# Optimization experiments

Hardware: AMD Instinct MI355X
Metric: run time of the kernel (lower is better)

## Reference

```python
import jax, jax.numpy as jnp
import numpy as np
from jax import lax

S, B, W = 128, 64, 16          # sent_len, batch, word_len
V, CV = 50000, 100             # word vocab, char vocab
WE, CE, FN, CK = 300, 30, 4, 3 # word emb dim, char emb dim, char filter num, char kernel
C = 512                        # cnn_out_channel
NT = 20                        # number of tags
NL = 3                         # number of GLU conv layers
PAD = 0


def setup_inputs() -> dict:
    key = jax.random.key(0)
    ks = jax.random.split(key, 16)
    words = jax.random.randint(ks[0], (S, B), 1, V)          # no pads -> full CRF mask
    chars = jax.random.randint(ks[1], (B, S, W), 1, CV)
    tags = jax.random.randint(ks[2], (S, B), 0, NT)
    word_emb = jax.random.normal(ks[3], (V, WE), jnp.float32) * 0.1
    char_emb = jax.random.normal(ks[4], (CV, CE), jnp.float32) * 0.1
    char_cnn_w = jax.random.normal(ks[5], (CE * FN, 1, CK), jnp.float32) * 0.1  # grouped conv, groups=CE
    char_cnn_b = jax.random.normal(ks[6], (CE * FN,), jnp.float32) * 0.01
    lin_w = jax.random.normal(ks[7], (WE + CE * FN, C), jnp.float32) * 0.05
    lin_b = jax.random.normal(ks[8], (C,), jnp.float32) * 0.01
    conv_w = jax.random.normal(ks[9], (NL, 2 * C, C, 3), jnp.float32) * 0.03
    conv_b = jax.random.normal(ks[10], (NL, 2 * C), jnp.float32) * 0.01
    fc_w = jax.random.normal(ks[11], (C, NT), jnp.float32) * 0.05
    fc_b = jax.random.normal(ks[12], (NT,), jnp.float32) * 0.01
    crf_start = jax.random.normal(ks[13], (NT,), jnp.float32) * 0.1
    crf_end = jax.random.normal(ks[14], (NT,), jnp.float32) * 0.1
    crf_trans = jax.random.normal(ks[15], (NT, NT), jnp.float32) * 0.1
    return dict(words=words, chars=chars, tags=tags, word_emb=word_emb, char_emb=char_emb,
                char_cnn_w=char_cnn_w, char_cnn_b=char_cnn_b, lin_w=lin_w, lin_b=lin_b,
                conv_w=conv_w, conv_b=conv_b, fc_w=fc_w, fc_b=fc_b,
                crf_start=crf_start, crf_end=crf_end, crf_trans=crf_trans)


def _emissions(words, chars, word_emb, char_emb, char_cnn_w, char_cnn_b,
               lin_w, lin_b, conv_w, conv_b, fc_w, fc_b):
    s, b = words.shape
    # word embeddings: [S,B,WE]
    emb_out = word_emb[words]
    # char embeddings + batched grouped char-CNN (replaces the python loop over sent positions)
    ch = char_emb[chars]                                   # [B,S,W,CE]
    ch = ch.reshape(b * s, W, CE).transpose(0, 2, 1)       # [B*S, CE, W]
    co = lax.conv_general_dilated(ch, char_cnn_w, (1,), 'VALID',
                                  dimension_numbers=('NCH', 'OIH', 'NCH'),
                                  feature_group_count=CE)
    co = co + char_cnn_b[None, :, None]                    # [B*S, CE*FN, W-CK+1]
    cf = co.max(axis=2).reshape(b, s, CE * FN).transpose(1, 0, 2)  # [S,B,120]
    word_features = jnp.concatenate([emb_out, cf], axis=2)  # [S,B,420]
    # gated-CNN (GLU) encoder
    h = word_features @ lin_w + lin_b                      # [S,B,C]
    h = jnp.transpose(h, (1, 2, 0))                        # [B,C,S]
    scale = jnp.sqrt(jnp.asarray(0.5, h.dtype))
    for l in range(conv_w.shape[0]):
        c = lax.conv_general_dilated(h, conv_w[l], (1,), ((1, 1),),
                                     dimension_numbers=('NCH', 'OIH', 'NCH'))
        c = c + conv_b[l][None, :, None]                   # [B,2C,S]
        a, g = jnp.split(c, 2, axis=1)
        h = (a * jax.nn.sigmoid(g) + h) * scale            # GLU + residual + scale
    enc = jnp.transpose(h, (2, 0, 1))                      # [S,B,C]
    emis = enc @ fc_w + fc_b                               # [S,B,NT]
    mask = (words != PAD)                                  # [S,B]
    return emis, mask


def _crf_nll(emis, tags, mask, crf_start, crf_end, crf_trans):
    s, b, nt = emis.shape
    maskf = mask.astype(emis.dtype)
    bi = jnp.arange(b)
    # numerator: score of the gold path
    emis_sc = jnp.take_along_axis(emis, tags[:, :, None], axis=2)[..., 0]  # [S,B]
    trans_sc = crf_trans[tags[:-1], tags[1:]]                              # [S-1,B]
    num = crf_start[tags[0]] + emis_sc[0] + ((trans_sc + emis_sc[1:]) * maskf[1:]).sum(0)
    last_idx = mask.sum(0).astype(jnp.int32) - 1
    num = num + crf_end[tags[last_idx, bi]]
    # denominator: forward algorithm (sequential DP over time)
    alpha0 = crf_start[None, :] + emis[0]                  # [B,NT]
    def step(alpha, xs):
        e_t, m_t = xs
        nxt = jax.nn.logsumexp(alpha[:, :, None] + crf_trans[None] + e_t[:, None, :], axis=1)
        return jnp.where(m_t[:, None], nxt, alpha), None
    alpha, _ = lax.scan(step, alpha0, (emis[1:], mask[1:]))
    logz = jax.nn.logsumexp(alpha + crf_end[None, :], axis=1)
    return -(num - logz).sum()


def _viterbi(emis, mask, crf_start, crf_end, crf_trans):
    s, b, nt = emis.shape
    bi = jnp.arange(b)
    ident = jnp.broadcast_to(jnp.arange(nt)[None, :], (b, nt))
    score0 = crf_start[None, :] + emis[0]                  # [B,NT]
    def step(score, xs):
        e_t, m_t = xs
        brd = score[:, :, None] + crf_trans[None]          # [B,NT_prev,NT_cur]
        bp = jnp.argmax(brd, axis=1)                       # [B,NT]
        nxt = jnp.max(brd, axis=1) + e_t
        score = jnp.where(m_t[:, None], nxt, score)
        bp = jnp.where(m_t[:, None], bp, ident)
        return score, bp
    final, bps = lax.scan(step, score0, (emis[1:], mask[1:]))  # bps [S-1,B,NT]
    last_tag = jnp.argmax(final + crf_end[None, :], axis=1)    # [B]
    def back(tag, bp):
        prev = bp[bi, tag]
        return prev, tag
    first_tag, rest = lax.scan(back, last_tag, bps, reverse=True)  # rest: tags at 1..S-1
    return jnp.concatenate([first_tag[None], rest], axis=0).astype(jnp.int32)  # [S,B]


def reference(words, chars, tags, word_emb, char_emb, char_cnn_w, char_cnn_b,
              lin_w, lin_b, conv_w, conv_b, fc_w, fc_b, crf_start, crf_end, crf_trans):
    emis, mask = _emissions(words, chars, word_emb, char_emb, char_cnn_w, char_cnn_b,
                            lin_w, lin_b, conv_w, conv_b, fc_w, fc_b)
    crf_out = _viterbi(emis, mask, crf_start, crf_end, crf_trans)
    crf_loss = _crf_nll(emis, tags, mask, crf_start, crf_end, crf_trans)
    return crf_out, crf_loss
```

## Files before the change

kernel.cpp:

```cpp
#include <hip/hip_runtime.h>
#include <math.h>

typedef unsigned short ushort_t;
typedef short bf16x8 __attribute__((ext_vector_type(8)));
typedef float f32x4 __attribute__((ext_vector_type(4)));
typedef unsigned short u16x8 __attribute__((ext_vector_type(8)));

#define S_ 128
#define B_ 64
#define W_ 16
#define CE_ 30
#define FN_ 4
#define WE_ 300
#define FEAT_ 420
#define C_ 512
#define NT_ 20
#define KL_ 448

#define LOG2E_ 1.44269504088896340736f
#define LN2_   0.69314718055994530942f

#define WF_OFF   0
#define EM_OFF   3440640
#define NLL_OFF  3604480
#define H0_OFF   3604608
#define HBUF_F   2129920
#define H1_OFF   (H0_OFF + HBUF_F)
#define WS_OFF   (H1_OFF + HBUF_F)
#define WSP_F    2359296
#define LW_OFF   (WS_OFF + WSP_F)
#define FS_OFF   (LW_OFF + 114688)
#define FW_OFF   (FS_OFF + 1835008)
#define WLAYER   (1024*1536)

__device__ __forceinline__ float b2f(ushort_t h) {
    unsigned u = ((unsigned)h) << 16;
    float f; __builtin_memcpy(&f, &u, 4); return f;
}
__device__ __forceinline__ ushort_t f2b(float f) {
    unsigned u; __builtin_memcpy(&u, &f, 4);
    unsigned r = (u + 0x7FFFu + ((u >> 16) & 1u)) >> 16;
    return (ushort_t)r;
}
__device__ __forceinline__ void gload16(const void* g, void* l) {
    __builtin_amdgcn_global_load_lds((const __attribute__((address_space(1))) void*)g,
                                     (__attribute__((address_space(3))) void*)l,
                                     16, 0, 0);
}

__global__ void k_word_gather(const int* __restrict__ words,
                              const float* __restrict__ word_emb,
                              float* __restrict__ wf) {
    int n = blockIdx.x;
    int wid = words[n];
    int t = threadIdx.x;
    if (t < WE_ / 4) {
        const float4* src = (const float4*)(word_emb + (size_t)wid * WE_);
        float4* dst = (float4*)(wf + (size_t)n * FEAT_);
        dst[t] = src[t];
    }
}

__global__ void k_char_cnn(const int* __restrict__ chars,
                           const float* __restrict__ char_emb,
                           const float* __restrict__ cw,
                           const float* __restrict__ cb,
                           float* __restrict__ wf) {
    int n = blockIdx.x;
    int b = n >> 7;
    int s = n & 127;
    __shared__ int cidx[W_];
    int t = threadIdx.x;
    if (t < W_) cidx[t] = chars[n * W_ + t];
    __syncthreads();
    if (t < CE_ * FN_) {
        int g = t >> 2;
        float w0 = cw[t*3+0], w1 = cw[t*3+1], w2 = cw[t*3+2];
        float x[W_];
        #pragma unroll
        for (int j = 0; j < W_; ++j) x[j] = char_emb[cidx[j] * CE_ + g];
        float m = -INFINITY;
        #pragma unroll
        for (int j = 0; j < W_ - 2; ++j) {
            float v = x[j]*w0 + x[j+1]*w1 + x[j+2]*w2;
            m = fmaxf(m, v);
        }
        wf[(size_t)(s * B_ + b) * FEAT_ + WE_ + t] = m + cb[t];
    }
}

__global__ void k_split_w(const float* __restrict__ conv_w,
                          ushort_t* __restrict__ Wt) {
    size_t i = (size_t)blockIdx.x * 256 + threadIdx.x;
    int ci = (int)(i & 511);
    int kr = (int)((i >> 9) % 3);
    size_t lo_ = i / 1536;
    Wt[i] = f2b(conv_w[lo_ * 1536 + (size_t)ci * 3 + kr]);
}

__global__ void k_split_lw(const float* __restrict__ lin_w,
                           ushort_t* __restrict__ Lh) {
    int k = blockIdx.x;
    int c = threadIdx.x;
    float v = (k < FEAT_) ? lin_w[(size_t)k * C_ + c] : 0.f;
    Lh[(size_t)c * KL_ + k] = f2b(v);
}

__global__ void k_split_wf(const float* __restrict__ wf,
                           ushort_t* __restrict__ Fh) {
    int np = blockIdx.x;
    int b = np >> 7, s = np & 127;
    const float* src = wf + (size_t)(s * B_ + b) * FEAT_;
    int t = threadIdx.x;
    #pragma unroll
    for (int r = 0; r < 2; ++r) {
        int k = t + r * 224;
        float v = (k < FEAT_) ? src[k] : 0.f;
        Fh[(size_t)np * KL_ + k] = f2b(v);
    }
}

__global__ void k_split_fw(const float* __restrict__ fc_w, float* __restrict__ fwT) {
    int idx = blockIdx.x * 256 + threadIdx.x;
    if (idx < NT_ * C_) {
        int j = idx >> 9, c = idx & 511;
        fwT[idx] = fc_w[(size_t)c * NT_ + j];
    }
}

__global__ void k_zero_pad(ushort_t* b0, ushort_t* b1) {
    ushort_t* buf = blockIdx.y ? b1 : b0;
    int b = blockIdx.x;
    int t = threadIdx.x;
    unsigned* r0 = (unsigned*)(buf + ((size_t)b * 130 + 0) * 512);
    unsigned* r1 = (unsigned*)(buf + ((size_t)b * 130 + 129) * 512);
    r0[t] = 0u; r1[t] = 0u;
}

__global__ __launch_bounds__(256) void k_lin_gemm(
    const ushort_t* __restrict__ Lh, const ushort_t* __restrict__ Fh,
    const float* __restrict__ lb, ushort_t* __restrict__ Oh)
{
    __shared__ short lds[8192];
    short* AhS = lds;
    short* BhS = lds + 4096;

    const int bid = blockIdx.x;
    const int c0 = (bid & 3) << 7;
    const int n0 = (bid >> 2) << 7;
    const int t = threadIdx.x;
    const int w = t >> 6;
    const int lane = t & 63;
    const int wr = w >> 1, wc = w & 1;

    const int srow0 = (w << 5) + (lane >> 2);
    const int srow1 = srow0 + 16;
    const int j0 = (lane & 3) ^ ((srow0 >> 1) & 3);
    const int j1 = (lane & 3) ^ ((srow1 >> 1) & 3);
    const size_t aoff0 = (size_t)(c0 + srow0) * KL_ + j0 * 8;
    const size_t aoff1 = (size_t)(c0 + srow1) * KL_ + j1 * 8;
    const size_t boff0 = (size_t)(n0 + srow0) * KL_ + j0 * 8;
    const size_t boff1 = (size_t)(n0 + srow1) * KL_ + j1 * 8;
    const int wofs = w << 10;

    const int lr = lane & 15, kg = lane >> 4;
    int aro[4], bro[4];
    #pragma unroll
    for (int m = 0; m < 4; ++m) { int r = (wr << 6) + (m << 4) + lr; aro[m] = (r << 5) + ((kg ^ ((r >> 1) & 3)) << 3); }
    #pragma unroll
    for (int n = 0; n < 4; ++n) { int r = (wc << 6) + (n << 4) + lr; bro[n] = (r << 5) + ((kg ^ ((r >> 1) & 3)) << 3); }

    f32x4 acc[4][4];
    #pragma unroll
    for (int m = 0; m < 4; ++m)
        #pragma unroll
        for (int n = 0; n < 4; ++n) acc[m][n] = (f32x4){0.f, 0.f, 0.f, 0.f};

    for (int k0 = 0; k0 < KL_; k0 += 32) {
        gload16(Lh + aoff0 + k0, AhS + wofs);
        gload16(Lh + aoff1 + k0, AhS + wofs + 512);
        gload16(Fh + boff0 + k0, BhS + wofs);
        gload16(Fh + boff1 + k0, BhS + wofs + 512);
        __syncthreads();
        bf16x8 avh[4], bvh[4];
        #pragma unroll
        for (int m = 0; m < 4; ++m) avh[m] = *(const bf16x8*)(AhS + aro[m]);
        #pragma unroll
        for (int n = 0; n < 4; ++n) bvh[n] = *(const bf16x8*)(BhS + bro[n]);
        #pragma unroll
        for (int m = 0; m < 4; ++m)
            #pragma unroll
            for (int n = 0; n < 4; ++n)
                acc[m][n] = __builtin_amdgcn_mfma_f32_16x16x32_bf16(avh[m], bvh[n], acc[m][n], 0, 0, 0);
        __syncthreads();
    }

    #pragma unroll
    for (int m = 0; m < 4; ++m) {
        const int c = c0 + (wr << 6) + (m << 4) + (kg << 2);
        float4 bb = *(const float4*)(lb + c);
        #pragma unroll
        for (int n = 0; n < 4; ++n) {
            const int np = n0 + (wc << 6) + (n << 4) + lr;
            const int b = np >> 7, s = np & 127;
            ushort4 h4;
            h4.x = f2b(acc[m][n][0] + bb.x);
            h4.y = f2b(acc[m][n][1] + bb.y);
            h4.z = f2b(acc[m][n][2] + bb.z);
            h4.w = f2b(acc[m][n][3] + bb.w);
            *(ushort4*)(Oh + ((size_t)b * 130 + s + 1) * 512 + c) = h4;
        }
    }
}

__global__ __launch_bounds__(256) void k_conv_gemm(
    const ushort_t* __restrict__ Wt, const ushort_t* __restrict__ Ht,
    const float* __restrict__ cb,
    ushort_t* __restrict__ Ot)
{
    __shared__ short lds[17408];
    short* AS = lds;
    short* BS = lds + 12288;
    float* g_lds = (float*)lds;

    const int bid  = blockIdx.x;
    const int co0  = (bid & 7) << 6;
    const int b    = bid >> 3;
    const int t    = threadIdx.x;
    const int w    = t >> 6;
    const int lane = t & 63;
    const int wr   = w >> 1;
    const int wc   = w & 1;

    const int srow0 = (w << 5) + (lane >> 2);
    const int srow1 = srow0 + 16;
    const int j0 = (lane & 3) ^ ((srow0 >> 1) & 3);
    const int j1 = (lane & 3) ^ ((srow1 >> 1) & 3);
    const int coA0 = (srow0 < 64) ? (co0 + srow0) : (512 + co0 + srow0 - 64);
    const int coA1 = (srow1 < 64) ? (co0 + srow1) : (512 + co0 + srow1 - 64);
    const size_t aoff0 = (size_t)coA0 * 1536 + j0 * 8;
    const size_t aoff1 = (size_t)coA1 * 1536 + j1 * 8;
    const int lrow = lane >> 2;
    const int wofs = w << 10;

    const int lr = lane & 15, kg = lane >> 4;
    int aro[4];
    #pragma unroll
    for (int m = 0; m < 4; ++m) { int r = (wr << 6) + (m << 4) + lr; aro[m] = (r << 5) + ((kg ^ ((r >> 1) & 3)) << 3); }
    int bro[3][4];
    #pragma unroll
    for (int kr = 0; kr < 3; ++kr)
        #pragma unroll
        for (int n = 0; n < 4; ++n) {
            int r = (wc << 6) + (n << 4) + lr + kr;
            bro[kr][n] = (r << 5) + ((kg ^ ((r >> 1) & 3)) << 3);
        }

    f32x4 acc[4][4];
    #pragma unroll
    for (int m = 0; m < 4; ++m)
        #pragma unroll
        for (int n = 0; n < 4; ++n) acc[m][n] = (f32x4){0.f, 0.f, 0.f, 0.f};

    for (int ci0 = 0; ci0 < 512; ci0 += 32) {
        #pragma unroll
        for (int kr = 0; kr < 3; ++kr) {
            gload16(Wt + aoff0 + kr * 512 + ci0, AS + kr * 4096 + wofs);
            gload16(Wt + aoff1 + kr * 512 + ci0, AS + kr * 4096 + wofs + 512);
        }
        for (int i = w; i < 9; i += 4) {
            const int rr = (i << 4) + lrow;
            const int sl = (lane & 3) ^ ((rr >> 1) & 3);
            gload16(Ht + ((size_t)b * 130 + rr) * 512 + ci0 + sl * 8, BS + (i << 9));
        }
        __syncthreads();
        #pragma unroll
        for (int kr = 0; kr < 3; ++kr) {
            const short* A_h = AS + kr * 4096;
            bf16x8 avh[4], bvh[4];
            #pragma unroll
            for (int m = 0; m < 4; ++m) avh[m] = *(const bf16x8*)(A_h + aro[m]);
            #pragma unroll
            for (int n = 0; n < 4; ++n) bvh[n] = *(const bf16x8*)(BS + bro[kr][n]);
            #pragma unroll
            for (int m = 0; m < 4; ++m)
                #pragma unroll
                for (int n = 0; n < 4; ++n)
                    acc[m][n] = __builtin_amdgcn_mfma_f32_16x16x32_bf16(avh[m], bvh[n], acc[m][n], 0, 0, 0);
        }
        __syncthreads();
    }

    const float rs = 0.70710678118654752f;
    if (wr == 1) {
        #pragma unroll
        for (int m = 0; m < 4; ++m) {
            const int co_l = (m << 4) + (kg << 2);
            float4 bg = *(const float4*)(cb + 512 + co0 + co_l);
            #pragma unroll
            for (int n = 0; n < 4; ++n) {
                const int s_l = (wc << 6) + (n << 4) + lr;
                float4 gv;
                gv.x = acc[m][n][0] + bg.x;
                gv.y = acc[m][n][1] + bg.y;
                gv.z = acc[m][n][2] + bg.z;
                gv.w = acc[m][n][3] + bg.w;
                *(float4*)&g_lds[s_l * 68 + co_l] = gv;
            }
        }
    }
    __syncthreads();
    if (wr == 0) {
        #pragma unroll
        for (int m = 0; m < 4; ++m) {
            const int co_l = (m << 4) + (kg << 2);
            float4 ba = *(const float4*)(cb + co0 + co_l);
            #pragma unroll
            for (int n = 0; n < 4; ++n) {
                const int s_l = (wc << 6) + (n << 4) + lr;
                float4 gv = *(const float4*)&g_lds[s_l * 68 + co_l];
                size_t dst = ((size_t)b * 130 + s_l + 1) * 512 + co0 + co_l;
                ushort4 rh = *(const ushort4*)(Ht + dst);
                float a0 = acc[m][n][0] + ba.x, g0 = gv.x;
                float a1 = acc[m][n][1] + ba.y, g1 = gv.y;
                float a2 = acc[m][n][2] + ba.z, g2 = gv.z;
                float a3 = acc[m][n][3] + ba.w, g3 = gv.w;
                ushort4 h4;
                h4.x = f2b((a0 / (1.f + expf(-g0)) + b2f(rh.x)) * rs);
                h4.y = f2b((a1 / (1.f + expf(-g1)) + b2f(rh.y)) * rs);
                h4.z = f2b((a2 / (1.f + expf(-g2)) + b2f(rh.z)) * rs);
                h4.w = f2b((a3 / (1.f + expf(-g3)) + b2f(rh.w)) * rs);
                *(ushort4*)(Ot + dst) = h4;
            }
        }
    }
}

__global__ __launch_bounds__(256) void k_emis3(const ushort_t* __restrict__ hh,
                                               const float* __restrict__ fwT,
                                               const float* __restrict__ fc_b,
                                               float* __restrict__ emis) {
    __shared__ short hlds[16 * 520];
    __shared__ float wlds[20 * 516];
    const int b  = blockIdx.y;
    const int sc = blockIdx.x;
    const int t  = threadIdx.x;
    const int w  = t >> 6, lane = t & 63;

    #pragma unroll
    for (int i = 0; i < 4; ++i) {
        int r = w * 4 + i;
        gload16(hh + ((size_t)b * 130 + sc * 16 + r + 1) * 512 + lane * 8,
                hlds + r * 520);
    }
    for (int idx = t; idx < 20 * 128; idx += 256) {
        int j = idx >> 7, cq = (idx & 127) << 2;
        *(float4*)&wlds[j * 516 + cq] = *(const float4*)(fwT + j * 512 + cq);
    }
    __syncthreads();

    #pragma unroll
    for (int pass = 0; pass < 2; ++pass) {
        int slot = t + pass * 256;
        if (slot < 16 * NT_) {
            int r = slot / NT_, j = slot - r * NT_;
            const short* hp = hlds + r * 520;
            const float* wp = wlds + j * 516;
            float acc = 0.f;
            for (int c0 = 0; c0 < 512; c0 += 8) {
                u16x8 hv = *(const u16x8*)(hp + c0);
                float4 w0 = *(const float4*)(wp + c0);
                float4 w1 = *(const float4*)(wp + c0 + 4);
                acc += b2f(hv[0])*w0.x + b2f(hv[1])*w0.y + b2f(hv[2])*w0.z + b2f(hv[3])*w0.w
                     + b2f(hv[4])*w1.x + b2f(hv[5])*w1.y + b2f(hv[6])*w1.z + b2f(hv[7])*w1.w;
            }
            int s = sc * 16 + r;
            emis[((size_t)s * B_ + b) * NT_ + j] = acc + fc_b[j];
        }
    }
}

#define VMAX(a, b) __builtin_elementwise_max((a), (b))
#define MAX20T(mx, a0, a1, a2, a3, a4) \
    { f32x4 mv_ = VMAX(VMAX(VMAX(a0, a1), VMAX(a2, a3)), a4); \
      mx = fmaxf(fmaxf(mv_[0], mv_[1]), fmaxf(mv_[2], mv_[3])); }
#define SEL(ov, oi, av, ai, bv2, bi2) \
    { bool g_ = (bv2) > (av); ov = g_ ? (bv2) : (av); oi = g_ ? (bi2) : (ai); }
#define ARGMAX20(best, bi, v0, v1, v2, v3, v4) \
    { float p0v,p1v,p2v,p3v,p4v,p5v,p6v,p7v,p8v,p9v; \
      int   p0i,p1i,p2i,p3i,p4i,p5i,p6i,p7i,p8i,p9i; \
      SEL(p0v,p0i, v0[0],0,  v0[1],1);  SEL(p1v,p1i, v0[2],2,  v0[3],3); \
      SEL(p2v,p2i, v1[0],4,  v1[1],5);  SEL(p3v,p3i, v1[2],6,  v1[3],7); \
      SEL(p4v,p4i, v2[0],8,  v2[1],9);  SEL(p5v,p5i, v2[2],10, v2[3],11); \
      SEL(p6v,p6i, v3[0],12, v3[1],13); SEL(p7v,p7i, v3[2],14, v3[3],15); \
      SEL(p8v,p8i, v4[0],16, v4[1],17); SEL(p9v,p9i, v4[2],18, v4[3],19); \
      float q0v,q1v,q2v,q3v,q4v; int q0i,q1i,q2i,q3i,q4i; \
      SEL(q0v,q0i,p0v,p0i,p1v,p1i); SEL(q1v,q1i,p2v,p2i,p3v,p3i); \
      SEL(q2v,q2i,p4v,p4i,p5v,p5i); SEL(q3v,q3i,p6v,p6i,p7v,p7i); \
      SEL(q4v,q4i,p8v,p8i,p9v,p9i); \
      float r0v,r1v; int r0i,r1i; \
      SEL(r0v,r0i,q0v,q0i,q1v,q1i); SEL(r1v,r1i,q2v,q2i,q3v,q3i); \
      float s0v; int s0i; \
      SEL(s0v,s0i,r0v,r0i,r1v,r1i); \
      SEL(best,bi,s0v,s0i,q4v,q4i); }
#define EXPC(d, s) d[0]=__builtin_amdgcn_exp2f(s[0]*LOG2E_); d[1]=__builtin_amdgcn_exp2f(s[1]*LOG2E_); \
                   d[2]=__builtin_amdgcn_exp2f(s[2]*LOG2E_); d[3]=__builtin_amdgcn_exp2f(s[3]*LOG2E_)
#define LGKM0() asm volatile("s_waitcnt lgkmcnt(0)" ::: "memory")

__global__ __launch_bounds__(256) void k_crf(const float* __restrict__ emis,
                                             const int* __restrict__ words,
                                             const int* __restrict__ tags,
                                             const float* __restrict__ tstart,
                                             const float* __restrict__ tend,
                                             const float* __restrict__ ttrans,
                                             float* __restrict__ nll,
                                             float* __restrict__ out) {
    __shared__ float e_lds[S_ * NT_];
    __shared__ float pe_lds[S_ * NT_];
    __shared__ int   P_lds[S_ * NT_];
    __shared__ float brA[32], brB[32], brC[32], brD[32];
    __shared__ float Fv[NT_], Gv[NT_], a63[NT_], g63[NT_];
    __shared__ float CfL, CbL;
    __shared__ int tag63L;
    const int b = blockIdx.x;
    const int t = threadIdx.x;
    const int w = t >> 6;
    const int ln = t & 63;

    for (int idx = t; idx < S_ * NT_; idx += 256) {
        int tt = idx / NT_, j = idx - tt * NT_;
        float ev = emis[((size_t)tt * B_ + b) * NT_ + j];
        e_lds[idx] = ev;
        pe_lds[idx] = __builtin_amdgcn_exp2f(ev * LOG2E_);
    }
    __syncthreads();

    unsigned long long mlo = __ballot(words[ln * B_ + b] != 0);
    unsigned long long mhi = __ballot(words[(64 + ln) * B_ + b] != 0);
    const bool act = ln < NT_;
    const int jc = act ? ln : 0;
    float part = 0.f;

    #define MBIT(tt) ((((tt) < 64 ? (mlo >> (tt)) : (mhi >> ((tt) - 64))) & 1ull) != 0)

    if (w == 0) {
        for (int tt = ln; tt < S_; tt += 64) {
            int tgc = tags[tt * B_ + b];
            bool m = MBIT(tt);
            if (tt == 0) {
                part += tstart[tgc] + e_lds[tgc];
            } else if (m) {
                int tgp = tags[(tt - 1) * B_ + b];
                part += ttrans[tgp * NT_ + tgc] + e_lds[tt * NT_ + tgc];
            }
        }
        #pragma unroll
        for (int o = 32; o >= 1; o >>= 1) part += __shfl_down(part, o);

        f32x4 t0, t1, t2, t3, t4;
        #define LDTC(v, q) v = (f32x4){ ttrans[(4*(q)+0)*NT_ + jc], ttrans[(4*(q)+1)*NT_ + jc], \
                                        ttrans[(4*(q)+2)*NT_ + jc], ttrans[(4*(q)+3)*NT_ + jc] }
        LDTC(t0, 0); LDTC(t1, 1); LDTC(t2, 2); LDTC(t3, 3); LDTC(t4, 4);
        f32x4 E0, E1, E2, E3, E4;
        EXPC(E0, t0); EXPC(E1, t1); EXPC(E2, t2); EXPC(E3, t3); EXPC(E4, t4);

        float a0own = tstart[jc] + e_lds[jc];
        if (act) brA[ln] = a0own;
        LGKM0();
        f32x4 a0 = *(const f32x4*)&brA[0];
        f32x4 a1 = *(const f32x4*)&brA[4];
        f32x4 a2 = *(const f32x4*)&brA[8];
        f32x4 a3 = *(const f32x4*)&brA[12];
        f32x4 a4 = *(const f32x4*)&brA[16];
        float m0; MAX20T(m0, a0, a1, a2, a3, a4);
        float beta = __builtin_amdgcn_exp2f((a0own - m0) * LOG2E_);
        int L2 = 0;
        for (int tt = 1; tt < 64; ++tt) {
            if (MBIT(tt)) {
                float pe = pe_lds[tt * NT_ + jc];
                if (act) brA[ln] = beta;
                LGKM0();
                f32x4 b0 = *(const f32x4*)&brA[0];
                f32x4 b1 = *(const f32x4*)&brA[4];
                f32x4 b2 = *(const f32x4*)&brA[8];
                f32x4 b3 = *(const f32x4*)&brA[12];
                f32x4 b4 = *(const f32x4*)&brA[16];
                float mx; MAX20T(mx, b0, b1, b2, b3, b4);
                f32x4 pr = b0 * E0 + b1 * E1 + b2 * E2 + b3 * E3 + b4 * E4;
                float dot = (pr[0] + pr[1]) + (pr[2] + pr[3]);
                unsigned bits; __builtin_memcpy(&bits, &mx, 4);
                int ex = (int)((bits >> 23) & 255u) - 127;
                unsigned rb = (unsigned)(127 - ex) << 23;
                float r; __builtin_memcpy(&r, &rb, 4);
                L2 += ex;
                beta = dot * r * pe;
            }
        }
        if (act) Fv[ln] = beta;
        if (ln == 0) CfL = m0 + (float)L2 * LN2_;
    } else if (w == 1) {
        f32x4 r0, r1, r2, r3, r4;
        #define LDTR(v, q) v = (f32x4){ ttrans[jc*NT_ + 4*(q)+0], ttrans[jc*NT_ + 4*(q)+1], \
                                        ttrans[jc*NT_ + 4*(q)+2], ttrans[jc*NT_ + 4*(q)+3] }
        LDTR(r0, 0); LDTR(r1, 1); LDTR(r2, 2); LDTR(r3, 3); LDTR(r4, 4);
        f32x4 E0, E1, E2, E3, E4;
        EXPC(E0, r0); EXPC(E1, r1); EXPC(E2, r2); EXPC(E3, r3); EXPC(E4, r4);
        f32x4 d0 = (f32x4){ tend[0],  tend[1],  tend[2],  tend[3]  };
        f32x4 d1 = (f32x4){ tend[4],  tend[5],  tend[6],  tend[7]  };
        f32x4 d2 = (f32x4){ tend[8],  tend[9],  tend[10], tend[11] };
        f32x4 d3 = (f32x4){ tend[12], tend[13], tend[14], tend[15] };
        f32x4 d4 = (f32x4){ tend[16], tend[17], tend[18], tend[19] };
        float mend; MAX20T(mend, d0, d1, d2, d3, d4);
        float G = __builtin_amdgcn_exp2f((tend[jc] - mend) * LOG2E_);
        int L2b = 0;
        for (int tt = 126; tt >= 63; --tt) {
            if (MBIT(tt + 1)) {
                float w_own = G * pe_lds[(tt + 1) * NT_ + jc];
                if (act) brB[ln] = w_own;
                LGKM0();
                f32x4 q0 = *(const f32x4*)&brB[0];
                f32x4 q1 = *(const f32x4*)&brB[4];
                f32x4 q2 = *(const f32x4*)&brB[8];
                f32x4 q3 = *(const f32x4*)&brB[12];
                f32x4 q4 = *(const f32x4*)&brB[16];
                float mx; MAX20T(mx, q0, q1, q2, q3, q4);
                f32x4 pr = q0 * E0 + q1 * E1 + q2 * E2 + q3 * E3 + q4 * E4;
                float dot = (pr[0] + pr[1]) + (pr[2] + pr[3]);
                unsigned bits; __builtin_memcpy(&bits, &mx, 4);
                int ex = (int)((bits >> 23) & 255u) - 127;
                unsigned rb = (unsigned)(127 - ex) << 23;
                float r; __builtin_memcpy(&r, &rb, 4);
                L2b += ex;
                G = dot * r;
            }
        }
        if (act) Gv[ln] = G;
        if (ln == 0) CbL = mend + (float)L2b * LN2_;
    } else if (w == 2) {
        f32x4 t0, t1, t2, t3, t4;
        LDTC(t0, 0); LDTC(t1, 1); LDTC(t2, 2); LDTC(t3, 3); LDTC(t4, 4);
        float sown = tstart[jc] + e_lds[jc];
        if (act) brC[ln] = sown;
        LGKM0();
        for (int tt = 1; tt < 64; ++tt) {
            float e = e_lds[tt * NT_ + jc];
            f32x4 a0 = *(const f32x4*)&brC[0];
            f32x4 a1 = *(const f32x4*)&brC[4];
            f32x4 a2 = *(const f32x4*)&brC[8];
            f32x4 a3 = *(const f32x4*)&brC[12];
            f32x4 a4 = *(const f32x4*)&brC[16];
            f32x4 v0 = a0 + t0, v1 = a1 + t1, v2 = a2 + t2, v3 = a3 + t3, v4 = a4 + t4;
            float best; int bi;
            ARGMAX20(best, bi, v0, v1, v2, v3, v4);
            bool m = MBIT(tt);
            float nxt = best + e;
            sown = m ? nxt : sown;
            if (act) {
                brC[ln] = sown;
                P_lds[tt * NT_ + ln] = m ? bi : ln;
            }
            LGKM0();
        }
        if (act) a63[ln] = sown;
    } else {
        f32x4 r0, r1, r2, r3, r4;
        LDTR(r0, 0); LDTR(r1, 1); LDTR(r2, 2); LDTR(r3, 3); LDTR(r4, 4);
        float gown = tend[jc];
        if (act) brD[ln] = gown + e_lds[127 * NT_ + jc];
        LGKM0();
        for (int tt = 126; tt >= 63; --tt) {
            f32x4 q0 = *(const f32x4*)&brD[0];
            f32x4 q1 = *(const f32x4*)&brD[4];
            f32x4 q2 = *(const f32x4*)&brD[8];
            f32x4 q3 = *(const f32x4*)&brD[12];
            f32x4 q4 = *(const f32x4*)&brD[16];
            f32x4 v0 = r0 + q0, v1 = r1 + q1, v2 = r2 + q2, v3 = r3 + q3, v4 = r4 + q4;
            float best; int bi;
            ARGMAX20(best, bi, v0, v1, v2, v3, v4);
            bool m = MBIT(tt + 1);
            gown = m ? best : gown;
            if (act) {
                P_lds[(tt + 1) * NT_ + ln] = m ? bi : ln;
                brD[ln] = gown + e_lds[tt * NT_ + jc];
            }
            LGKM0();
        }
        if (act) g63[ln] = gown;
    }
    __syncthreads();

    if (t == 0) {
        float zf = 0.f;
        #pragma unroll
        for (int j = 0; j < NT_; ++j) zf += Fv[j] * Gv[j];
        float logz = CfL + CbL + __builtin_amdgcn_logf(zf) * LN2_;
        int cnt = __popcll(mlo) + __popcll(mhi);
        float num = part + tend[tags[(cnt - 1) * B_ + b]];
        nll[b] = logz - num;
        float bv = a63[0] + g63[0]; int bt = 0;
        #pragma unroll
        for (int j = 1; j < NT_; ++j) {
            float v = a63[j] + g63[j];
            if (v > bv) { bv = v; bt = j; }
        }
        tag63L = bt;
    }
    __syncthreads();

    if (t == 128) {
        int tag = tag63L;
        out[63 * B_ + b] = (float)tag;
        for (int tt = 63; tt >= 1; --tt) {
            tag = P_lds[tt * NT_ + tag];
            out[(tt - 1) * B_ + b] = (float)tag;
        }
    }
    if (t == 192) {
        int tag = tag63L;
        for (int tt = 64; tt < 128; ++tt) {
            tag = P_lds[tt * NT_ + tag];
            out[tt * B_ + b] = (float)tag;
        }
    }
}

__global__ void k_loss(const float* __restrict__ nll, float* __restrict__ out) {
    float v = nll[threadIdx.x];
    #pragma unroll
    for (int o = 32; o >= 1; o >>= 1) v += __shfl_down(v, o);
    if (threadIdx.x == 0) out[S_ * B_] = v;
}

extern "C" void kernel_launch(void* const* d_in, const int* in_sizes, int n_in,
                              void* d_out, int out_size, void* d_ws, size_t ws_size,
                              hipStream_t stream) {
    (void)in_sizes; (void)n_in; (void)out_size; (void)ws_size;
    const int*   words     = (const int*)d_in[0];
    const int*   chars     = (const int*)d_in[1];
    const int*   tags      = (const int*)d_in[2];
    const float* word_emb  = (const float*)d_in[3];
    const float* char_emb  = (const float*)d_in[4];
    const float* ccw       = (const float*)d_in[5];
    const float* ccb       = (const float*)d_in[6];
    const float* lin_w     = (const float*)d_in[7];
    const float* lin_b     = (const float*)d_in[8];
    const float* conv_w    = (const float*)d_in[9];
    const float* conv_b    = (const float*)d_in[10];
    const float* fc_w      = (const float*)d_in[11];
    const float* fc_b      = (const float*)d_in[12];
    const float* crf_start = (const float*)d_in[13];
    const float* crf_end   = (const float*)d_in[14];
    const float* crf_trans = (const float*)d_in[15];

    float* ws   = (float*)d_ws;
    float* wf   = ws + WF_OFF;
    float* em   = ws + EM_OFF;
    float* nll  = ws + NLL_OFF;
    ushort_t* h0  = (ushort_t*)(ws + H0_OFF);
    ushort_t* h1  = (ushort_t*)(ws + H1_OFF);
    ushort_t* wsp = (ushort_t*)(ws + WS_OFF);
    ushort_t* lwp = (ushort_t*)(ws + LW_OFF);
    ushort_t* fsp = (ushort_t*)(ws + FS_OFF);
    float* fwT  = ws + FW_OFF;
    float* out  = (float*)d_out;

    k_word_gather<<<S_ * B_, 128, 0, stream>>>(words, word_emb, wf);
    k_char_cnn<<<B_ * S_, 128, 0, stream>>>(chars, char_emb, ccw, ccb, wf);
    k_split_w<<<18432, 256, 0, stream>>>(conv_w, wsp);
    k_split_lw<<<KL_, 512, 0, stream>>>(lin_w, lwp);
    k_split_wf<<<S_ * B_, 224, 0, stream>>>(wf, fsp);
    k_split_fw<<<40, 256, 0, stream>>>(fc_w, fwT);
    k_lin_gemm<<<256, 256, 0, stream>>>(lwp, fsp, lin_b, h0);
    k_zero_pad<<<dim3(64, 2), 256, 0, stream>>>(h0, h1);

    k_conv_gemm<<<512, 256, 0, stream>>>(wsp,              h0, conv_b,        h1);
    k_conv_gemm<<<512, 256, 0, stream>>>(wsp + WLAYER,     h1, conv_b + 1024, h0);
    k_conv_gemm<<<512, 256, 0, stream>>>(wsp + 2*WLAYER,   h0, conv_b + 2048, h1);

    k_emis3<<<dim3(8, B_), 256, 0, stream>>>(h1, fwT, fc_b, em);
    k_crf<<<B_, 256, 0, stream>>>(em, words, tags, crf_start, crf_end, crf_trans, nll, out);
    k_loss<<<1, 64, 0, stream>>>(nll, out);
}
```

Baseline: 192.6 us.

## Fuse feature bf16 packing into gathers and double batch per conv block

The word-gather and char-CNN kernels now write bf16 features directly into the padded GEMM input layout. This removes the fp32 intermediate buffer and the separate split kernel along with its extra memory round-trip. The GLU conv GEMM now processes two batch rows per block with 512 threads (8 waves), so each weight tile loaded into LDS is reused across twice as many sequence positions, and the grid is halved to 256 blocks. The trade-off is larger LDS use and fewer blocks, which may reduce occupancy or leave CUs idle on a 256-CU part.

```diff
diff --git a/kernel.cpp b/kernel.cpp
--- a/kernel.cpp
+++ b/kernel.cpp
@@ -20,10 +20,9 @@
 #define LOG2E_ 1.44269504088896340736f
 #define LN2_   0.69314718055994530942f
 
-#define WF_OFF   0
-#define EM_OFF   3440640
-#define NLL_OFF  3604480
-#define H0_OFF   3604608
+#define EM_OFF   0
+#define NLL_OFF  163840
+#define H0_OFF   163968
 #define HBUF_F   2129920
 #define H1_OFF   (H0_OFF + HBUF_F)
 #define WS_OFF   (H1_OFF + HBUF_F)
@@ -50,14 +49,17 @@
 
 __global__ void k_word_gather(const int* __restrict__ words,
                               const float* __restrict__ word_emb,
-                              float* __restrict__ wf) {
+                              ushort_t* __restrict__ Fh) {
     int n = blockIdx.x;
+    int s = n >> 6, b = n & 63;
+    int np = b * 128 + s;
     int wid = words[n];
     int t = threadIdx.x;
     if (t < WE_ / 4) {
-        const float4* src = (const float4*)(word_emb + (size_t)wid * WE_);
-        float4* dst = (float4*)(wf + (size_t)n * FEAT_);
-        dst[t] = src[t];
+        float4 v = ((const float4*)(word_emb + (size_t)wid * WE_))[t];
+        ushort4 o;
+        o.x = f2b(v.x); o.y = f2b(v.y); o.z = f2b(v.z); o.w = f2b(v.w);
+        *(ushort4*)(Fh + (size_t)np * KL_ + t * 4) = o;
     }
 }
 
@@ -65,10 +67,11 @@
                            const float* __restrict__ char_emb,
                            const float* __restrict__ cw,
                            const float* __restrict__ cb,
-                           float* __restrict__ wf) {
+                           ushort_t* __restrict__ Fh) {
     int n = blockIdx.x;
     int b = n >> 7;
     int s = n & 127;
+    int np = b * 128 + s;
     __shared__ int cidx[W_];
     int t = threadIdx.x;
     if (t < W_) cidx[t] = chars[n * W_ + t];
@@ -85,8 +88,9 @@
             float v = x[j]*w0 + x[j+1]*w1 + x[j+2]*w2;
             m = fmaxf(m, v);
         }
-        wf[(size_t)(s * B_ + b) * FEAT_ + WE_ + t] = m + cb[t];
-    }
+        Fh[(size_t)np * KL_ + WE_ + t] = f2b(m + cb[t]);
+    }
+    if (t < KL_ - FEAT_) Fh[(size_t)np * KL_ + FEAT_ + t] = 0;
 }
 
 __global__ void k_split_w(const float* __restrict__ conv_w,
@@ -104,20 +108,6 @@
     int c = threadIdx.x;
     float v = (k < FEAT_) ? lin_w[(size_t)k * C_ + c] : 0.f;
     Lh[(size_t)c * KL_ + k] = f2b(v);
-}
-
-__global__ void k_split_wf(const float* __restrict__ wf,
-                           ushort_t* __restrict__ Fh) {
-    int np = blockIdx.x;
-    int b = np >> 7, s = np & 127;
-    const float* src = wf + (size_t)(s * B_ + b) * FEAT_;
-    int t = threadIdx.x;
-    #pragma unroll
-    for (int r = 0; r < 2; ++r) {
-        int k = t + r * 224;
-        float v = (k < FEAT_) ? src[k] : 0.f;
-        Fh[(size_t)np * KL_ + k] = f2b(v);
-    }
 }
 
 __global__ void k_split_fw(const float* __restrict__ fc_w, float* __restrict__ fwT) {
@@ -213,47 +203,43 @@
     }
 }
 
-__global__ __launch_bounds__(256) void k_conv_gemm(
+__global__ __launch_bounds__(512) void k_conv_gemm(
     const ushort_t* __restrict__ Wt, const ushort_t* __restrict__ Ht,
     const float* __restrict__ cb,
     ushort_t* __restrict__ Ot)
 {
-    __shared__ short lds[17408];
-    short* AS = lds;
-    short* BS = lds + 12288;
-    float* g_lds = (float*)lds;
+    __shared__ float g_lds[4 * 64 * 68];
+    short* AS = (short*)g_lds;
+    short* BS = AS + 12288;
 
     const int bid  = blockIdx.x;
     const int co0  = (bid & 7) << 6;
-    const int b    = bid >> 3;
+    const int b0   = (bid >> 3) << 1;
     const int t    = threadIdx.x;
     const int w    = t >> 6;
     const int lane = t & 63;
-    const int wr   = w >> 1;
-    const int wc   = w & 1;
-
-    const int srow0 = (w << 5) + (lane >> 2);
-    const int srow1 = srow0 + 16;
-    const int j0 = (lane & 3) ^ ((srow0 >> 1) & 3);
-    const int j1 = (lane & 3) ^ ((srow1 >> 1) & 3);
-    const int coA0 = (srow0 < 64) ? (co0 + srow0) : (512 + co0 + srow0 - 64);
-    const int coA1 = (srow1 < 64) ? (co0 + srow1) : (512 + co0 + srow1 - 64);
-    const size_t aoff0 = (size_t)coA0 * 1536 + j0 * 8;
-    const size_t aoff1 = (size_t)coA1 * 1536 + j1 * 8;
+    const int wr   = w >> 2;
+    const int wc   = w & 3;
+
+    const int srow = (w << 4) + (lane >> 2);
+    const int jA = (lane & 3) ^ ((srow >> 1) & 3);
+    const int coA = (srow < 64) ? (co0 + srow) : (512 + co0 + srow - 64);
+    const size_t aoff = (size_t)coA * 1536 + jA * 8;
     const int lrow = lane >> 2;
-    const int wofs = w << 10;
 
     const int lr = lane & 15, kg = lane >> 4;
     int aro[4];
     #pragma unroll
     for (int m = 0; m < 4; ++m) { int r = (wr << 6) + (m << 4) + lr; aro[m] = (r << 5) + ((kg ^ ((r >> 1) & 3)) << 3); }
     int bro[3][4];
+    const int slab = wc >> 1;
+    const int s_off = (wc & 1) << 6;
     #pragma unroll
     for (int kr = 0; kr < 3; ++kr)
         #pragma unroll
         for (int n = 0; n < 4; ++n) {
-            int r = (wc << 6) + (n << 4) + lr + kr;
-            bro[kr][n] = (r << 5) + ((kg ^ ((r >> 1) & 3)) << 3);
+            int r = s_off + (n << 4) + lr + kr;
+            bro[kr][n] = slab * 4608 + (r << 5) + ((kg ^ ((r >> 1) & 3)) << 3);
         }
 
     f32x4 acc[4][4];
@@ -264,14 +250,14 @@
 
     for (int ci0 = 0; ci0 < 512; ci0 += 32) {
         #pragma unroll
-        for (int kr = 0; kr < 3; ++kr) {
-            gload16(Wt + aoff0 + kr * 512 + ci0, AS + kr * 4096 + wofs);
-            gload16(Wt + aoff1 + kr * 512 + ci0, AS + kr * 4096 + wofs + 512);
-        }
-        for (int i = w; i < 9; i += 4) {
-            const int rr = (i << 4) + lrow;
-            const int sl = (lane & 3) ^ ((rr >> 1) & 3);
-            gload16(Ht + ((size_t)b * 130 + rr) * 512 + ci0 + sl * 8, BS + (i << 9));
+        for (int kr = 0; kr < 3; ++kr)
+            gload16(Wt + aoff + kr * 512 + ci0, AS + kr * 4096 + (w << 9));
+        for (int i = w; i < 18; i += 8) {
+            const int sl2 = i / 9, grp = i - sl2 * 9;
+            const int rr = (grp << 4) + lrow;
+            const int sj = (lane & 3) ^ ((rr >> 1) & 3);
+            gload16(Ht + ((size_t)(b0 + sl2) * 130 + rr) * 512 + ci0 + sj * 8,
+                    BS + sl2 * 4608 + (grp << 9));
         }
         __syncthreads();
         #pragma unroll
@@ -299,27 +285,29 @@
             float4 bg = *(const float4*)(cb + 512 + co0 + co_l);
             #pragma unroll
             for (int n = 0; n < 4; ++n) {
-                const int s_l = (wc << 6) + (n << 4) + lr;
+                const int seg_s = (n << 4) + lr;
                 float4 gv;
                 gv.x = acc[m][n][0] + bg.x;
                 gv.y = acc[m][n][1] + bg.y;
                 gv.z = acc[m][n][2] + bg.z;
                 gv.w = acc[m][n][3] + bg.w;
-                *(float4*)&g_lds[s_l * 68 + co_l] = gv;
+                *(float4*)&g_lds[((wc << 6) + seg_s) * 68 + co_l] = gv;
             }
         }
     }
     __syncthreads();
     if (wr == 0) {
+        const int bb = b0 + (wc >> 1);
         #pragma unroll
         for (int m = 0; m < 4; ++m) {
             const int co_l = (m << 4) + (kg << 2);
             float4 ba = *(const float4*)(cb + co0 + co_l);
             #pragma unroll
             for (int n = 0; n < 4; ++n) {
-                const int s_l = (wc << 6) + (n << 4) + lr;
-                float4 gv = *(const float4*)&g_lds[s_l * 68 + co_l];
-                size_t dst = ((size_t)b * 130 + s_l + 1) * 512 + co0 + co_l;
+                const int seg_s = (n << 4) + lr;
+                float4 gv = *(const float4*)&g_lds[((wc << 6) + seg_s) * 68 + co_l];
+                const int s_g = s_off + seg_s;
+                size_t dst = ((size_t)bb * 130 + s_g + 1) * 512 + co0 + co_l;
                 ushort4 rh = *(const ushort4*)(Ht + dst);
                 float a0 = acc[m][n][0] + ba.x, g0 = gv.x;
                 float a1 = acc[m][n][1] + ba.y, g1 = gv.y;
@@ -653,7 +641,6 @@
     const float* crf_trans = (const float*)d_in[15];
 
     float* ws   = (float*)d_ws;
-    float* wf   = ws + WF_OFF;
     float* em   = ws + EM_OFF;
     float* nll  = ws + NLL_OFF;
     ushort_t* h0  = (ushort_t*)(ws + H0_OFF);
@@ -664,18 +651,17 @@
     float* fwT  = ws + FW_OFF;
     float* out  = (float*)d_out;
 
-    k_word_gather<<<S_ * B_, 128, 0, stream>>>(words, word_emb, wf);
-    k_char_cnn<<<B_ * S_, 128, 0, stream>>>(chars, char_emb, ccw, ccb, wf);
+    k_word_gather<<<S_ * B_, 128, 0, stream>>>(words, word_emb, fsp);
+    k_char_cnn<<<B_ * S_, 128, 0, stream>>>(chars, char_emb, ccw, ccb, fsp);
     k_split_w<<<18432, 256, 0, stream>>>(conv_w, wsp);
     k_split_lw<<<KL_, 512, 0, stream>>>(lin_w, lwp);
-    k_split_wf<<<S_ * B_, 224, 0, stream>>>(wf, fsp);
     k_split_fw<<<40, 256, 0, stream>>>(fc_w, fwT);
     k_lin_gemm<<<256, 256, 0, stream>>>(lwp, fsp, lin_b, h0);
     k_zero_pad<<<dim3(64, 2), 256, 0, stream>>>(h0, h1);
 
-    k_conv_gemm<<<512, 256, 0, stream>>>(wsp,              h0, conv_b,        h1);
-    k_conv_gemm<<<512, 256, 0, stream>>>(wsp + WLAYER,     h1, conv_b + 1024, h0);
-    k_conv_gemm<<<512, 256, 0, stream>>>(wsp + 2*WLAYER,   h0, conv_b + 2048, h1);
+    k_conv_gemm<<<256, 512, 0, stream>>>(wsp,              h0, conv_b,        h1);
+    k_conv_gemm<<<256, 512, 0, stream>>>(wsp + WLAYER,     h1, conv_b + 1024, h0);
+    k_conv_gemm<<<256, 512, 0, stream>>>(wsp + 2*WLAYER,   h0, conv_b + 2048, h1);
 
     k_emis3<<<dim3(8, B_), 256, 0, stream>>>(h1, fwT, fc_b, em);
     k_crf<<<B_, 256, 0, stream>>>(em, words, tags, crf_start, crf_end, crf_trans, nll, out);
```

Measured after the change: 194.3 us. About the same (+0.9%).

## Double-buffer conv GEMM LDS tiles and write bf16 features directly

Applied to the files above, without the earlier changes.

The conv GEMM now prefetches the next K-slice of weights and activations into a second LDS buffer while MFMAs run on the current one, so global-load latency overlaps with compute. Separately, the word-gather and char-CNN kernels write bf16 features straight into the padded GEMM input, which removes the fp32 intermediate buffer and the k_split_wf pass. Doubling LDS per block to about 66KB may reduce occupancy.

```diff
diff --git a/kernel.cpp b/kernel.cpp
--- a/kernel.cpp
+++ b/kernel.cpp
@@ -20,10 +20,9 @@
 #define LOG2E_ 1.44269504088896340736f
 #define LN2_   0.69314718055994530942f
 
-#define WF_OFF   0
-#define EM_OFF   3440640
-#define NLL_OFF  3604480
-#define H0_OFF   3604608
+#define EM_OFF   0
+#define NLL_OFF  163840
+#define H0_OFF   163968
 #define HBUF_F   2129920
 #define H1_OFF   (H0_OFF + HBUF_F)
 #define WS_OFF   (H1_OFF + HBUF_F)
@@ -50,14 +49,17 @@
 
 __global__ void k_word_gather(const int* __restrict__ words,
                               const float* __restrict__ word_emb,
-                              float* __restrict__ wf) {
+                              ushort_t* __restrict__ Fh) {
     int n = blockIdx.x;
+    int s = n >> 6, b = n & 63;
+    int np = b * 128 + s;
     int wid = words[n];
     int t = threadIdx.x;
     if (t < WE_ / 4) {
-        const float4* src = (const float4*)(word_emb + (size_t)wid * WE_);
-        float4* dst = (float4*)(wf + (size_t)n * FEAT_);
-        dst[t] = src[t];
+        float4 v = ((const float4*)(word_emb + (size_t)wid * WE_))[t];
+        ushort4 o;
+        o.x = f2b(v.x); o.y = f2b(v.y); o.z = f2b(v.z); o.w = f2b(v.w);
+        *(ushort4*)(Fh + (size_t)np * KL_ + t * 4) = o;
     }
 }
 
@@ -65,10 +67,11 @@
                            const float* __restrict__ char_emb,
                            const float* __restrict__ cw,
                            const float* __restrict__ cb,
-                           float* __restrict__ wf) {
+                           ushort_t* __restrict__ Fh) {
     int n = blockIdx.x;
     int b = n >> 7;
     int s = n & 127;
+    int np = b * 128 + s;
     __shared__ int cidx[W_];
     int t = threadIdx.x;
     if (t < W_) cidx[t] = chars[n * W_ + t];
@@ -85,8 +88,9 @@
             float v = x[j]*w0 + x[j+1]*w1 + x[j+2]*w2;
             m = fmaxf(m, v);
         }
-        wf[(size_t)(s * B_ + b) * FEAT_ + WE_ + t] = m + cb[t];
-    }
+        Fh[(size_t)np * KL_ + WE_ + t] = f2b(m + cb[t]);
+    }
+    if (t < KL_ - FEAT_) Fh[(size_t)np * KL_ + FEAT_ + t] = 0;
 }
 
 __global__ void k_split_w(const float* __restrict__ conv_w,
@@ -104,20 +108,6 @@
     int c = threadIdx.x;
     float v = (k < FEAT_) ? lin_w[(size_t)k * C_ + c] : 0.f;
     Lh[(size_t)c * KL_ + k] = f2b(v);
-}
-
-__global__ void k_split_wf(const float* __restrict__ wf,
-                           ushort_t* __restrict__ Fh) {
-    int np = blockIdx.x;
-    int b = np >> 7, s = np & 127;
-    const float* src = wf + (size_t)(s * B_ + b) * FEAT_;
-    int t = threadIdx.x;
-    #pragma unroll
-    for (int r = 0; r < 2; ++r) {
-        int k = t + r * 224;
-        float v = (k < FEAT_) ? src[k] : 0.f;
-        Fh[(size_t)np * KL_ + k] = f2b(v);
-    }
 }
 
 __global__ void k_split_fw(const float* __restrict__ fc_w, float* __restrict__ fwT) {
@@ -213,15 +203,14 @@
     }
 }
 
+#define CBUFS 16896
 __global__ __launch_bounds__(256) void k_conv_gemm(
     const ushort_t* __restrict__ Wt, const ushort_t* __restrict__ Ht,
     const float* __restrict__ cb,
     ushort_t* __restrict__ Ot)
 {
-    __shared__ short lds[17408];
-    short* AS = lds;
-    short* BS = lds + 12288;
-    float* g_lds = (float*)lds;
+    __shared__ short lds2[2 * CBUFS];
+    float* g_lds = (float*)lds2;
 
     const int bid  = blockIdx.x;
     const int co0  = (bid & 7) << 6;
@@ -262,18 +251,41 @@
         #pragma unroll
         for (int n = 0; n < 4; ++n) acc[m][n] = (f32x4){0.f, 0.f, 0.f, 0.f};
 
-    for (int ci0 = 0; ci0 < 512; ci0 += 32) {
+    {
+        short* AS = lds2;
+        short* BS = lds2 + 12288;
         #pragma unroll
         for (int kr = 0; kr < 3; ++kr) {
-            gload16(Wt + aoff0 + kr * 512 + ci0, AS + kr * 4096 + wofs);
-            gload16(Wt + aoff1 + kr * 512 + ci0, AS + kr * 4096 + wofs + 512);
+            gload16(Wt + aoff0 + kr * 512, AS + kr * 4096 + wofs);
+            gload16(Wt + aoff1 + kr * 512, AS + kr * 4096 + wofs + 512);
         }
         for (int i = w; i < 9; i += 4) {
             const int rr = (i << 4) + lrow;
-            const int sl = (lane & 3) ^ ((rr >> 1) & 3);
-            gload16(Ht + ((size_t)b * 130 + rr) * 512 + ci0 + sl * 8, BS + (i << 9));
-        }
-        __syncthreads();
+            const int sj = (lane & 3) ^ ((rr >> 1) & 3);
+            gload16(Ht + ((size_t)b * 130 + rr) * 512 + sj * 8, BS + (i << 9));
+        }
+    }
+    __syncthreads();
+
+    for (int it = 0; it < 16; ++it) {
+        const int cur = it & 1;
+        if (it + 1 < 16) {
+            const int ci0 = (it + 1) << 5;
+            short* ASn = lds2 + (cur ^ 1) * CBUFS;
+            short* BSn = ASn + 12288;
+            #pragma unroll
+            for (int kr = 0; kr < 3; ++kr) {
+                gload16(Wt + aoff0 + kr * 512 + ci0, ASn + kr * 4096 + wofs);
+                gload16(Wt + aoff1 + kr * 512 + ci0, ASn + kr * 4096 + wofs + 512);
+            }
+            for (int i = w; i < 9; i += 4) {
+                const int rr = (i << 4) + lrow;
+                const int sj = (lane & 3) ^ ((rr >> 1) & 3);
+                gload16(Ht + ((size_t)b * 130 + rr) * 512 + ci0 + sj * 8, BSn + (i << 9));
+            }
+        }
+        const short* AS = lds2 + cur * CBUFS;
+        const short* BS = AS + 12288;
         #pragma unroll
         for (int kr = 0; kr < 3; ++kr) {
             const short* A_h = AS + kr * 4096;
@@ -653,7 +665,6 @@
     const float* crf_trans = (const float*)d_in[15];
 
     float* ws   = (float*)d_ws;
-    float* wf   = ws + WF_OFF;
     float* em   = ws + EM_OFF;
     float* nll  = ws + NLL_OFF;
     ushort_t* h0  = (ushort_t*)(ws + H0_OFF);
@@ -664,11 +675,10 @@
     float* fwT  = ws + FW_OFF;
     float* out  = (float*)d_out;
 
-    k_word_gather<<<S_ * B_, 128, 0, stream>>>(words, word_emb, wf);
-    k_char_cnn<<<B_ * S_, 128, 0, stream>>>(chars, char_emb, ccw, ccb, wf);
+    k_word_gather<<<S_ * B_, 128, 0, stream>>>(words, word_emb, fsp);
+    k_char_cnn<<<B_ * S_, 128, 0, stream>>>(chars, char_emb, ccw, ccb, fsp);
     k_split_w<<<18432, 256, 0, stream>>>(conv_w, wsp);
     k_split_lw<<<KL_, 512, 0, stream>>>(lin_w, lwp);
-    k_split_wf<<<S_ * B_, 224, 0, stream>>>(wf, fsp);
     k_split_fw<<<40, 256, 0, stream>>>(fc_w, fwT);
     k_lin_gemm<<<256, 256, 0, stream>>>(lwp, fsp, lin_b, h0);
     k_zero_pad<<<dim3(64, 2), 256, 0, stream>>>(h0, h1);
```

New measurement: 185.2 us. -3.9%, faster.
